# Kernel tuning notes

Measured on AMD Instinct MI355X. Metric: run time of the kernel, lower is better.

## Reference

```python
import jax, jax.numpy as jnp
import numpy as np

N_NODES = 50000


def _gcn_norm(edge_index, num_nodes):
    # PyG GCNConv default: add self-loops, symmetric normalization D^-1/2 A D^-1/2
    src, dst = edge_index[0], edge_index[1]
    loops = jnp.arange(num_nodes, dtype=src.dtype)
    src = jnp.concatenate([src, loops])
    dst = jnp.concatenate([dst, loops])
    deg = jax.ops.segment_sum(jnp.ones_like(src, dtype=jnp.float32), dst,
                              num_segments=num_nodes)
    dis = jnp.where(deg > 0, jax.lax.rsqrt(jnp.maximum(deg, 1.0)), 0.0)
    norm = dis[src] * dis[dst]  # [E']
    return src, dst, norm


def _gcn_conv(x, W, b, src, dst, norm, num_nodes):
    h = x @ W                                   # [N, out] transform first
    msg = h[src] * norm[:, None]                # [E', out] gather + scale
    agg = jax.ops.segment_sum(msg, dst, num_segments=num_nodes)  # scatter-add
    return agg + b


def setup_inputs() -> dict:
    key = jax.random.key(0)
    k1, k2, k3, k4 = jax.random.split(key, 4)
    n, e, d_in, d_h = N_NODES, 800000, 256, 128
    basic_block = jax.random.normal(k1, (n, d_in), dtype=jnp.float32)
    edge_index = jax.random.randint(k2, (2, e), 0, n, dtype=jnp.int64)
    W1 = jax.random.normal(k3, (d_in, d_h), dtype=jnp.float32) * (1.0 / np.sqrt(d_in))
    b1 = jnp.zeros((d_h,), dtype=jnp.float32)
    W2 = jax.random.normal(k4, (d_h, d_h), dtype=jnp.float32) * (1.0 / np.sqrt(d_h))
    b2 = jnp.zeros((d_h,), dtype=jnp.float32)
    return {"basic_block": basic_block, "edge_index": edge_index,
            "W1": W1, "b1": b1, "W2": W2, "b2": b2}


def reference(basic_block, edge_index, W1, b1, W2, b2):
    n = basic_block.shape[0]
    src, dst, norm = _gcn_norm(edge_index, n)
    x = jax.nn.relu(_gcn_conv(basic_block, W1, b1, src, dst, norm, n))
    x = _gcn_conv(x, W2, b2, src, dst, norm, n)
    return x
```

## Files before the change

### kernel.cpp

```cpp
#include <hip/hip_runtime.h>
#include <hip/hip_bf16.h>
#include <stdint.h>

#define D_H 128

typedef __bf16 bf16_t;
typedef unsigned short u16;
typedef bf16_t bf16x8 __attribute__((ext_vector_type(8)));
typedef bf16_t bf16x4 __attribute__((ext_vector_type(4)));
typedef float  f32x4  __attribute__((ext_vector_type(4)));

__global__ void k_countrank(const int* __restrict__ dst, int* __restrict__ cnt,
                            u16* __restrict__ rank, int E, int crBlocks,
                            const float* __restrict__ W1, bf16_t* __restrict__ W1h,
                            bf16_t* __restrict__ W1l, int K1,
                            const float* __restrict__ W2, bf16_t* __restrict__ W2h,
                            bf16_t* __restrict__ W2l, int K2) {
    if ((int)blockIdx.x < crBlocks) {
        int e = blockIdx.x * 256 + threadIdx.x;
        if (e < E) rank[e] = (u16)atomicAdd(&cnt[dst[e]], 1);
        return;
    }
    int id = ((int)blockIdx.x - crBlocks) * 256 + threadIdx.x;
    int n1 = K1 * 128;
    if (id < n1) {
        int k = id >> 7, n = id & 127;
        float w = W1[id];
        bf16_t h = (bf16_t)w;
        W1h[(size_t)n * K1 + k] = h;
        W1l[(size_t)n * K1 + k] = (bf16_t)(w - (float)h);
    } else if (id < n1 + K2 * 128) {
        int id2 = id - n1;
        int k = id2 >> 7, n = id2 & 127;
        float w = W2[id2];
        bf16_t h = (bf16_t)w;
        W2h[(size_t)n * K2 + k] = h;
        W2l[(size_t)n * K2 + k] = (bf16_t)(w - (float)h);
    }
}

__global__ __launch_bounds__(1024) void k_scan1(const int* __restrict__ cnt,
                                                int* __restrict__ out,
                                                int* __restrict__ bsums,
                                                float* __restrict__ dis, int N) {
    __shared__ int tmp[1024];
    int t = threadIdx.x;
    int i = blockIdx.x * 1024 + t;
    int v = (i < N) ? cnt[i] : 0;
    if (i < N) dis[i] = 1.0f / sqrtf((float)(v + 1));
    tmp[t] = v;
    __syncthreads();
    for (int d = 1; d < 1024; d <<= 1) {
        int x = (t >= d) ? tmp[t - d] : 0;
        __syncthreads();
        tmp[t] += x;
        __syncthreads();
    }
    if (i < N) out[i] = tmp[t] - v;
    if (t == 1023) bsums[blockIdx.x] = tmp[t];
}

__global__ void k_scan2(int* __restrict__ bsums, int nb) {
    __shared__ int tmp[64];
    int t = threadIdx.x;
    int v = (t < nb) ? bsums[t] : 0;
    tmp[t] = v;
    __syncthreads();
    for (int d = 1; d < 64; d <<= 1) {
        int x = (t >= d) ? tmp[t - d] : 0;
        __syncthreads();
        tmp[t] += x;
        __syncthreads();
    }
    if (t < nb) bsums[t] = tmp[t] - v;
}

__global__ __launch_bounds__(1024) void k_scan3(int* __restrict__ off,
                                                const int* __restrict__ bsums,
                                                int N, int E) {
    int i = blockIdx.x * 1024 + threadIdx.x;
    if (i < N) off[i] += bsums[blockIdx.x];
    if (i == 0) off[N] = E;
}

#define LDK 40
#define FILL_PER 2

__global__ __launch_bounds__(256) void k_mm1fill(
        const float* __restrict__ Af,
        const bf16_t* __restrict__ Wh, const bf16_t* __restrict__ Wl,
        const float* __restrict__ dis, bf16_t* __restrict__ Cb,
        int N, int K,
        const int* __restrict__ src, const int* __restrict__ dst,
        const int* __restrict__ off, const u16* __restrict__ rank,
        u16* __restrict__ csr16, int E, int totThreads) {
    __shared__ bf16_t AsH[64][LDK];
    __shared__ bf16_t AsL[64][LDK];
    __shared__ bf16_t BsH[64][LDK];
    __shared__ bf16_t BsL[64][LDK];

    const int t    = threadIdx.x;
    const int lane = t & 63;
    const int wave = t >> 6;
    const int row0 = ((int)blockIdx.x >> 1) * 64;
    const int col0 = ((int)blockIdx.x & 1) * 64;
    const int wm   = (wave & 1) * 32;
    const int wn   = (wave >> 1) * 32;
    const int fm   = lane & 15;
    const int fq   = lane >> 4;

    const int g = (int)blockIdx.x * 256 + t;
    int epos[FILL_PER];
    u16 esrc[FILL_PER];
#pragma unroll
    for (int i = 0; i < FILL_PER; i++) {
        int e = g + i * totThreads;
        if (e < E) {
            int d = dst[e];
            epos[i] = off[d] + (int)rank[e];
            esrc[i] = (u16)src[e];
        } else {
            epos[i] = -1;
            esrc[i] = 0;
        }
    }

    const int ar0 = t >> 3;
    const int ar1 = (t >> 3) + 32;
    const int ac4 = t & 7;
    const int br  = t >> 2;
    const int bc8 = t & 3;
    const int gr0 = row0 + ar0;
    const int gr1 = row0 + ar1;

    float4 rA0, rA1;
    bf16x8 rBh, rBl;
    const float4 fz = make_float4(0.f, 0.f, 0.f, 0.f);

    auto gload = [&](int k0) {
        rA0 = (gr0 < N) ? *(const float4*)(Af + (size_t)gr0 * K + k0 + ac4 * 4) : fz;
        rA1 = (gr1 < N) ? *(const float4*)(Af + (size_t)gr1 * K + k0 + ac4 * 4) : fz;
        rBh = *(const bf16x8*)(Wh + (size_t)(col0 + br) * K + k0 + bc8 * 8);
        rBl = *(const bf16x8*)(Wl + (size_t)(col0 + br) * K + k0 + bc8 * 8);
    };
    auto lstore = [&]() {
        float4 v = rA0;
        bf16_t h0 = (bf16_t)v.x, h1 = (bf16_t)v.y, h2 = (bf16_t)v.z, h3 = (bf16_t)v.w;
        *(bf16x4*)&AsH[ar0][ac4 * 4] = (bf16x4){h0, h1, h2, h3};
        *(bf16x4*)&AsL[ar0][ac4 * 4] = (bf16x4){(bf16_t)(v.x - (float)h0), (bf16_t)(v.y - (float)h1),
                                                (bf16_t)(v.z - (float)h2), (bf16_t)(v.w - (float)h3)};
        v = rA1;
        h0 = (bf16_t)v.x; h1 = (bf16_t)v.y; h2 = (bf16_t)v.z; h3 = (bf16_t)v.w;
        *(bf16x4*)&AsH[ar1][ac4 * 4] = (bf16x4){h0, h1, h2, h3};
        *(bf16x4*)&AsL[ar1][ac4 * 4] = (bf16x4){(bf16_t)(v.x - (float)h0), (bf16_t)(v.y - (float)h1),
                                                (bf16_t)(v.z - (float)h2), (bf16_t)(v.w - (float)h3)};
        *(bf16x8*)&BsH[br][bc8 * 8] = rBh;
        *(bf16x8*)&BsL[br][bc8 * 8] = rBl;
    };

    f32x4 acc[2][2] = {};

    gload(0);
    for (int k0 = 0; k0 < K; k0 += 32) {
        __syncthreads();
        lstore();
        if (k0 + 32 < K) gload(k0 + 32);
        __syncthreads();

        bf16x8 ah[2], al[2], bh[2], bl[2];
#pragma unroll
        for (int i = 0; i < 2; i++) {
            ah[i] = *(const bf16x8*)&AsH[wm + i * 16 + fm][fq * 8];
            al[i] = *(const bf16x8*)&AsL[wm + i * 16 + fm][fq * 8];
            bh[i] = *(const bf16x8*)&BsH[wn + i * 16 + fm][fq * 8];
            bl[i] = *(const bf16x8*)&BsL[wn + i * 16 + fm][fq * 8];
        }
#pragma unroll
        for (int mi = 0; mi < 2; mi++)
#pragma unroll
            for (int ni = 0; ni < 2; ni++) {
                acc[mi][ni] = __builtin_amdgcn_mfma_f32_16x16x32_bf16(ah[mi], bh[ni], acc[mi][ni], 0, 0, 0);
                acc[mi][ni] = __builtin_amdgcn_mfma_f32_16x16x32_bf16(ah[mi], bl[ni], acc[mi][ni], 0, 0, 0);
                acc[mi][ni] = __builtin_amdgcn_mfma_f32_16x16x32_bf16(al[mi], bh[ni], acc[mi][ni], 0, 0, 0);
            }
    }

#pragma unroll
    for (int mi = 0; mi < 2; mi++)
#pragma unroll
        for (int r = 0; r < 4; r++) {
            int grow = row0 + wm + mi * 16 + fq * 4 + r;
            if (grow < N) {
                float dr = dis[grow];
#pragma unroll
                for (int ni = 0; ni < 2; ni++)
                    Cb[(size_t)grow * D_H + col0 + wn + ni * 16 + fm] = (bf16_t)(dr * acc[mi][ni][r]);
            }
        }

#pragma unroll
    for (int i = 0; i < FILL_PER; i++)
        if (epos[i] >= 0) csr16[epos[i]] = esrc[i];
}

__global__ __launch_bounds__(256) void k_mm2(const bf16_t* __restrict__ Ah,
                                             const bf16_t* __restrict__ Al,
                                             const bf16_t* __restrict__ Wh,
                                             const bf16_t* __restrict__ Wl,
                                             const float* __restrict__ dis,
                                             bf16_t* __restrict__ Cb,
                                             int N, int K) {
    __shared__ bf16_t AsH[64][LDK];
    __shared__ bf16_t AsL[64][LDK];
    __shared__ bf16_t BsH[64][LDK];
    __shared__ bf16_t BsL[64][LDK];

    const int t    = threadIdx.x;
    const int lane = t & 63;
    const int wave = t >> 6;
    const int row0 = ((int)blockIdx.x >> 1) * 64;
    const int col0 = ((int)blockIdx.x & 1) * 64;
    const int wm   = (wave & 1) * 32;
    const int wn   = (wave >> 1) * 32;
    const int fm   = lane & 15;
    const int fq   = lane >> 4;

    const int r8  = t >> 2;
    const int c8  = t & 3;
    const int gr  = row0 + r8;

    bf16x8 rAh, rAl, rBh, rBl;
    auto gload = [&](int k0) {
        bf16x8 z = {};
        rAh = (gr < N) ? *(const bf16x8*)(Ah + (size_t)gr * K + k0 + c8 * 8) : z;
        rAl = (gr < N) ? *(const bf16x8*)(Al + (size_t)gr * K + k0 + c8 * 8) : z;
        rBh = *(const bf16x8*)(Wh + (size_t)(col0 + r8) * K + k0 + c8 * 8);
        rBl = *(const bf16x8*)(Wl + (size_t)(col0 + r8) * K + k0 + c8 * 8);
    };
    auto lstore = [&]() {
        *(bf16x8*)&AsH[r8][c8 * 8] = rAh;
        *(bf16x8*)&AsL[r8][c8 * 8] = rAl;
        *(bf16x8*)&BsH[r8][c8 * 8] = rBh;
        *(bf16x8*)&BsL[r8][c8 * 8] = rBl;
    };

    f32x4 acc[2][2] = {};

    gload(0);
    for (int k0 = 0; k0 < K; k0 += 32) {
        __syncthreads();
        lstore();
        if (k0 + 32 < K) gload(k0 + 32);
        __syncthreads();

        bf16x8 ah[2], al[2], bh[2], bl[2];
#pragma unroll
        for (int i = 0; i < 2; i++) {
            ah[i] = *(const bf16x8*)&AsH[wm + i * 16 + fm][fq * 8];
            al[i] = *(const bf16x8*)&AsL[wm + i * 16 + fm][fq * 8];
            bh[i] = *(const bf16x8*)&BsH[wn + i * 16 + fm][fq * 8];
            bl[i] = *(const bf16x8*)&BsL[wn + i * 16 + fm][fq * 8];
        }
#pragma unroll
        for (int mi = 0; mi < 2; mi++)
#pragma unroll
            for (int ni = 0; ni < 2; ni++) {
                acc[mi][ni] = __builtin_amdgcn_mfma_f32_16x16x32_bf16(ah[mi], bh[ni], acc[mi][ni], 0, 0, 0);
                acc[mi][ni] = __builtin_amdgcn_mfma_f32_16x16x32_bf16(ah[mi], bl[ni], acc[mi][ni], 0, 0, 0);
                acc[mi][ni] = __builtin_amdgcn_mfma_f32_16x16x32_bf16(al[mi], bh[ni], acc[mi][ni], 0, 0, 0);
            }
    }

#pragma unroll
    for (int mi = 0; mi < 2; mi++)
#pragma unroll
        for (int r = 0; r < 4; r++) {
            int grow = row0 + wm + mi * 16 + fq * 4 + r;
            if (grow < N) {
                float dr = dis[grow];
#pragma unroll
                for (int ni = 0; ni < 2; ni++)
                    Cb[(size_t)grow * D_H + col0 + wn + ni * 16 + fm] = (bf16_t)(dr * acc[mi][ni][r]);
            }
        }
}

__global__ __launch_bounds__(256) void k_agg(const bf16_t* __restrict__ Hb,
                                             const float* __restrict__ dis,
                                             const int* __restrict__ off,
                                             const u16* __restrict__ csr16,
                                             const float4* __restrict__ bias4,
                                             float4* __restrict__ outF,
                                             bf16_t* __restrict__ outH,
                                             bf16_t* __restrict__ outL,
                                             int N, int mode) {
    const int slot = threadIdx.x >> 4;
    const int lane = threadIdx.x & 15;
    const int node = blockIdx.x * 16 + slot;
    if (node >= N) return;

    const bf16_t* Hrow = Hb + (size_t)lane * 8;

    float a0[8], a1[8], a2[8], a3[8];
    {
        bf16x8 v = *(const bf16x8*)(Hrow + (size_t)node * D_H);
#pragma unroll
        for (int j = 0; j < 8; j++) { a0[j] = (float)v[j]; a1[j] = 0.f; a2[j] = 0.f; a3[j] = 0.f; }
    }

    int p  = off[node];
    int p1 = off[node + 1];

    for (; p + 4 <= p1; p += 4) {
        int s0 = (int)csr16[p + 0], s1 = (int)csr16[p + 1];
        int s2 = (int)csr16[p + 2], s3 = (int)csr16[p + 3];
        bf16x8 h0 = *(const bf16x8*)(Hrow + (size_t)s0 * D_H);
        bf16x8 h1 = *(const bf16x8*)(Hrow + (size_t)s1 * D_H);
        bf16x8 h2 = *(const bf16x8*)(Hrow + (size_t)s2 * D_H);
        bf16x8 h3 = *(const bf16x8*)(Hrow + (size_t)s3 * D_H);
#pragma unroll
        for (int j = 0; j < 8; j++) {
            a0[j] += (float)h0[j];
            a1[j] += (float)h1[j];
            a2[j] += (float)h2[j];
            a3[j] += (float)h3[j];
        }
    }
    if (p + 2 <= p1) {
        int s0 = (int)csr16[p + 0], s1 = (int)csr16[p + 1];
        bf16x8 h0 = *(const bf16x8*)(Hrow + (size_t)s0 * D_H);
        bf16x8 h1 = *(const bf16x8*)(Hrow + (size_t)s1 * D_H);
#pragma unroll
        for (int j = 0; j < 8; j++) { a0[j] += (float)h0[j]; a1[j] += (float)h1[j]; }
        p += 2;
    }
    if (p < p1) {
        int s0 = (int)csr16[p];
        bf16x8 h0 = *(const bf16x8*)(Hrow + (size_t)s0 * D_H);
#pragma unroll
        for (int j = 0; j < 8; j++) a2[j] += (float)h0[j];
    }

    float sum[8];
#pragma unroll
    for (int j = 0; j < 8; j++) sum[j] = (a0[j] + a1[j]) + (a2[j] + a3[j]);

    const float  di = dis[node];
    const float4 b0 = bias4[lane * 2];
    const float4 b1 = bias4[lane * 2 + 1];
    float v0 = fmaf(di, sum[0], b0.x), v1 = fmaf(di, sum[1], b0.y);
    float v2 = fmaf(di, sum[2], b0.z), v3 = fmaf(di, sum[3], b0.w);
    float v4 = fmaf(di, sum[4], b1.x), v5 = fmaf(di, sum[5], b1.y);
    float v6 = fmaf(di, sum[6], b1.z), v7 = fmaf(di, sum[7], b1.w);

    if (mode == 1) {
        v0 = fmaxf(v0, 0.f); v1 = fmaxf(v1, 0.f); v2 = fmaxf(v2, 0.f); v3 = fmaxf(v3, 0.f);
        v4 = fmaxf(v4, 0.f); v5 = fmaxf(v5, 0.f); v6 = fmaxf(v6, 0.f); v7 = fmaxf(v7, 0.f);
        bf16_t h0 = (bf16_t)v0, h1 = (bf16_t)v1, h2 = (bf16_t)v2, h3 = (bf16_t)v3;
        bf16_t h4 = (bf16_t)v4, h5 = (bf16_t)v5, h6 = (bf16_t)v6, h7 = (bf16_t)v7;
        *(bf16x8*)(outH + (size_t)node * D_H + lane * 8) =
            (bf16x8){h0, h1, h2, h3, h4, h5, h6, h7};
        *(bf16x8*)(outL + (size_t)node * D_H + lane * 8) =
            (bf16x8){(bf16_t)(v0 - (float)h0), (bf16_t)(v1 - (float)h1),
                     (bf16_t)(v2 - (float)h2), (bf16_t)(v3 - (float)h3),
                     (bf16_t)(v4 - (float)h4), (bf16_t)(v5 - (float)h5),
                     (bf16_t)(v6 - (float)h6), (bf16_t)(v7 - (float)h7)};
    } else {
        outF[(size_t)node * 32 + lane * 2]     = make_float4(v0, v1, v2, v3);
        outF[(size_t)node * 32 + lane * 2 + 1] = make_float4(v4, v5, v6, v7);
    }
}

extern "C" void kernel_launch(void* const* d_in, const int* in_sizes, int n_in,
                              void* d_out, int out_size, void* d_ws, size_t ws_size,
                              hipStream_t stream) {
    const float* X  = (const float*)d_in[0];
    const int*   ei = (const int*)d_in[1];
    const float* W1 = (const float*)d_in[2];
    const float* b1 = (const float*)d_in[3];
    const float* W2 = (const float*)d_in[4];
    const float* b2 = (const float*)d_in[5];
    float* out = (float*)d_out;

    const int N  = in_sizes[0] / 256;
    const int E  = in_sizes[1] / 2;
    const int K1 = 256;

    const int* src = ei;
    const int* dst = ei + E;

    uintptr_t p = (uintptr_t)d_ws;
    auto carve = [&](size_t bytes) {
        uintptr_t q = p;
        p += (bytes + 255) & ~(size_t)255;
        return q;
    };
    int*    cnt   = (int*)carve((size_t)N * 4);
    int*    off   = (int*)carve((size_t)(N + 1) * 4);
    int*    bsums = (int*)carve(64 * 4);
    float*  dis   = (float*)carve((size_t)N * 4);
    u16*    rank  = (u16*)carve((size_t)E * 2);
    u16*    csr16 = (u16*)carve((size_t)E * 2);
    bf16_t* Hb    = (bf16_t*)carve((size_t)N * D_H * 2);
    bf16_t* X1h   = (bf16_t*)carve((size_t)N * D_H * 2);
    bf16_t* X1l   = (bf16_t*)carve((size_t)N * D_H * 2);
    bf16_t* W1h   = (bf16_t*)carve((size_t)K1 * D_H * 2);
    bf16_t* W1l   = (bf16_t*)carve((size_t)K1 * D_H * 2);
    bf16_t* W2h   = (bf16_t*)carve((size_t)D_H * D_H * 2);
    bf16_t* W2l   = (bf16_t*)carve((size_t)D_H * D_H * 2);

    const int nb = (N + 1023) / 1024;

    hipMemsetAsync(cnt, 0, (size_t)N * 4, stream);
    const int gcr   = (E + 255) / 256;
    const int gprep = (K1 * 128 + D_H * 128 + 255) / 256;
    k_countrank<<<gcr + gprep, 256, 0, stream>>>(dst, cnt, rank, E, gcr,
                                                 W1, W1h, W1l, K1,
                                                 W2, W2h, W2l, D_H);
    k_scan1<<<nb, 1024, 0, stream>>>(cnt, off, bsums, dis, N);
    k_scan2<<<1, 64, 0, stream>>>(bsums, nb);
    k_scan3<<<nb, 1024, 0, stream>>>(off, bsums, N, E);

    const int gmm = ((N + 63) / 64) * 2;
    const int gag = (N + 15) / 16;

    k_mm1fill<<<gmm, 256, 0, stream>>>(X, W1h, W1l, dis, Hb, N, K1,
                                       src, dst, off, rank, csr16, E, gmm * 256);
    k_agg<<<gag, 256, 0, stream>>>(Hb, dis, off, csr16,
                                   (const float4*)b1, nullptr, X1h, X1l, N, 1);

    k_mm2<<<gmm, 256, 0, stream>>>(X1h, X1l, W2h, W2l, dis, Hb, N, D_H);
    k_agg<<<gag, 256, 0, stream>>>(Hb, dis, off, csr16,
                                   (const float4*)b2, (float4*)out, nullptr, nullptr, N, 0);
}
```

Measured before the change: 269.5 us.

## Split degree counters into four copies and drop register prefetch in GEMMs

Spreads the edge-degree atomics across four counter copies, selected by block index, so atomics on the same node contend less. The scan sums the four copies, and a per-copy offset table is built so the CSR fill can place each edge correctly. Separately, both GEMM kernels drop register double-buffering of the global tiles and now load straight into LDS each iteration, which lowers register pressure but no longer overlaps the loads with compute. The cost is extra memory traffic for the memset and the offset arrays, plus an additional offset table.

```diff
diff --git a/kernel.cpp b/kernel.cpp
--- a/kernel.cpp
+++ b/kernel.cpp
@@ -10,18 +10,22 @@
 typedef bf16_t bf16x4 __attribute__((ext_vector_type(4)));
 typedef float  f32x4  __attribute__((ext_vector_type(4)));
 
-__global__ void k_countrank(const int* __restrict__ dst, int* __restrict__ cnt,
-                            u16* __restrict__ rank, int E, int crBlocks,
-                            const float* __restrict__ W1, bf16_t* __restrict__ W1h,
-                            bf16_t* __restrict__ W1l, int K1,
-                            const float* __restrict__ W2, bf16_t* __restrict__ W2h,
-                            bf16_t* __restrict__ W2l, int K2) {
-    if ((int)blockIdx.x < crBlocks) {
-        int e = blockIdx.x * 256 + threadIdx.x;
-        if (e < E) rank[e] = (u16)atomicAdd(&cnt[dst[e]], 1);
+__global__ void k_pre(const int* __restrict__ dst, int* __restrict__ cnt4,
+                      u16* __restrict__ rank, int E, int Nn, int gcr,
+                      const float* __restrict__ W1, bf16_t* __restrict__ W1h,
+                      bf16_t* __restrict__ W1l, int K1,
+                      const float* __restrict__ W2, bf16_t* __restrict__ W2h,
+                      bf16_t* __restrict__ W2l, int K2) {
+    int bx = (int)blockIdx.x;
+    if (bx < gcr) {
+        int e = bx * 256 + threadIdx.x;
+        if (e < E) {
+            int d = dst[e];
+            rank[e] = (u16)atomicAdd(&cnt4[(bx & 3) * Nn + d], 1);
+        }
         return;
     }
-    int id = ((int)blockIdx.x - crBlocks) * 256 + threadIdx.x;
+    int id = (bx - gcr) * 256 + threadIdx.x;
     int n1 = K1 * 128;
     if (id < n1) {
         int k = id >> 7, n = id & 127;
@@ -39,15 +43,18 @@
     }
 }
 
-__global__ __launch_bounds__(1024) void k_scan1(const int* __restrict__ cnt,
+__global__ __launch_bounds__(1024) void k_scan1(const int* __restrict__ cnt4,
                                                 int* __restrict__ out,
                                                 int* __restrict__ bsums,
                                                 float* __restrict__ dis, int N) {
     __shared__ int tmp[1024];
     int t = threadIdx.x;
     int i = blockIdx.x * 1024 + t;
-    int v = (i < N) ? cnt[i] : 0;
-    if (i < N) dis[i] = 1.0f / sqrtf((float)(v + 1));
+    int v = 0;
+    if (i < N) {
+        v = cnt4[i] + cnt4[N + i] + cnt4[2 * N + i] + cnt4[3 * N + i];
+        dis[i] = 1.0f / sqrtf((float)(v + 1));
+    }
     tmp[t] = v;
     __syncthreads();
     for (int d = 1; d < 1024; d <<= 1) {
@@ -77,9 +84,19 @@
 
 __global__ __launch_bounds__(1024) void k_scan3(int* __restrict__ off,
                                                 const int* __restrict__ bsums,
+                                                const int* __restrict__ cnt4,
+                                                int* __restrict__ offc,
                                                 int N, int E) {
     int i = blockIdx.x * 1024 + threadIdx.x;
-    if (i < N) off[i] += bsums[blockIdx.x];
+    if (i < N) {
+        int o = off[i] + bsums[blockIdx.x];
+        off[i] = o;
+        int c0 = cnt4[i], c1 = cnt4[N + i], c2 = cnt4[2 * N + i];
+        offc[i]         = o;
+        offc[N + i]     = o + c0;
+        offc[2 * N + i] = o + c0 + c1;
+        offc[3 * N + i] = o + c0 + c1 + c2;
+    }
     if (i == 0) off[N] = E;
 }
 
@@ -92,7 +109,7 @@
         const float* __restrict__ dis, bf16_t* __restrict__ Cb,
         int N, int K,
         const int* __restrict__ src, const int* __restrict__ dst,
-        const int* __restrict__ off, const u16* __restrict__ rank,
+        const int* __restrict__ offc, const u16* __restrict__ rank,
         u16* __restrict__ csr16, int E, int totThreads) {
     __shared__ bf16_t AsH[64][LDK];
     __shared__ bf16_t AsL[64][LDK];
@@ -116,8 +133,9 @@
     for (int i = 0; i < FILL_PER; i++) {
         int e = g + i * totThreads;
         if (e < E) {
-            int d = dst[e];
-            epos[i] = off[d] + (int)rank[e];
+            int d    = dst[e];
+            int copy = (e >> 8) & 3;
+            epos[i] = offc[copy * N + d] + (int)rank[e];
             esrc[i] = (u16)src[e];
         } else {
             epos[i] = -1;
@@ -125,46 +143,32 @@
         }
     }
 
-    const int ar0 = t >> 3;
-    const int ar1 = (t >> 3) + 32;
-    const int ac4 = t & 7;
-    const int br  = t >> 2;
-    const int bc8 = t & 3;
-    const int gr0 = row0 + ar0;
-    const int gr1 = row0 + ar1;
-
-    float4 rA0, rA1;
-    bf16x8 rBh, rBl;
-    const float4 fz = make_float4(0.f, 0.f, 0.f, 0.f);
-
-    auto gload = [&](int k0) {
-        rA0 = (gr0 < N) ? *(const float4*)(Af + (size_t)gr0 * K + k0 + ac4 * 4) : fz;
-        rA1 = (gr1 < N) ? *(const float4*)(Af + (size_t)gr1 * K + k0 + ac4 * 4) : fz;
-        rBh = *(const bf16x8*)(Wh + (size_t)(col0 + br) * K + k0 + bc8 * 8);
-        rBl = *(const bf16x8*)(Wl + (size_t)(col0 + br) * K + k0 + bc8 * 8);
-    };
-    auto lstore = [&]() {
-        float4 v = rA0;
-        bf16_t h0 = (bf16_t)v.x, h1 = (bf16_t)v.y, h2 = (bf16_t)v.z, h3 = (bf16_t)v.w;
-        *(bf16x4*)&AsH[ar0][ac4 * 4] = (bf16x4){h0, h1, h2, h3};
-        *(bf16x4*)&AsL[ar0][ac4 * 4] = (bf16x4){(bf16_t)(v.x - (float)h0), (bf16_t)(v.y - (float)h1),
-                                                (bf16_t)(v.z - (float)h2), (bf16_t)(v.w - (float)h3)};
-        v = rA1;
-        h0 = (bf16_t)v.x; h1 = (bf16_t)v.y; h2 = (bf16_t)v.z; h3 = (bf16_t)v.w;
-        *(bf16x4*)&AsH[ar1][ac4 * 4] = (bf16x4){h0, h1, h2, h3};
-        *(bf16x4*)&AsL[ar1][ac4 * 4] = (bf16x4){(bf16_t)(v.x - (float)h0), (bf16_t)(v.y - (float)h1),
-                                                (bf16_t)(v.z - (float)h2), (bf16_t)(v.w - (float)h3)};
-        *(bf16x8*)&BsH[br][bc8 * 8] = rBh;
-        *(bf16x8*)&BsL[br][bc8 * 8] = rBl;
-    };
-
     f32x4 acc[2][2] = {};
 
-    gload(0);
     for (int k0 = 0; k0 < K; k0 += 32) {
         __syncthreads();
-        lstore();
-        if (k0 + 32 < K) gload(k0 + 32);
+#pragma unroll
+        for (int i = 0; i < 2; i++) {
+            int idx = t + i * 256;
+            int r   = idx >> 3;
+            int c4  = idx & 7;
+            int gr  = row0 + r;
+            float4 v = make_float4(0.f, 0.f, 0.f, 0.f);
+            if (gr < N) v = *(const float4*)(Af + (size_t)gr * K + k0 + c4 * 4);
+            bf16_t h0 = (bf16_t)v.x, h1 = (bf16_t)v.y, h2 = (bf16_t)v.z, h3 = (bf16_t)v.w;
+            bf16_t l0 = (bf16_t)(v.x - (float)h0);
+            bf16_t l1 = (bf16_t)(v.y - (float)h1);
+            bf16_t l2 = (bf16_t)(v.z - (float)h2);
+            bf16_t l3 = (bf16_t)(v.w - (float)h3);
+            *(bf16x4*)&AsH[r][c4 * 4] = (bf16x4){h0, h1, h2, h3};
+            *(bf16x4*)&AsL[r][c4 * 4] = (bf16x4){l0, l1, l2, l3};
+        }
+        {
+            int r  = t >> 2;
+            int c8 = t & 3;
+            *(bf16x8*)&BsH[r][c8 * 8] = *(const bf16x8*)(Wh + (size_t)(col0 + r) * K + k0 + c8 * 8);
+            *(bf16x8*)&BsL[r][c8 * 8] = *(const bf16x8*)(Wl + (size_t)(col0 + r) * K + k0 + c8 * 8);
+        }
         __syncthreads();
 
         bf16x8 ah[2], al[2], bh[2], bl[2];
@@ -225,32 +229,24 @@
     const int fm   = lane & 15;
     const int fq   = lane >> 4;
 
-    const int r8  = t >> 2;
-    const int c8  = t & 3;
-    const int gr  = row0 + r8;
-
-    bf16x8 rAh, rAl, rBh, rBl;
-    auto gload = [&](int k0) {
-        bf16x8 z = {};
-        rAh = (gr < N) ? *(const bf16x8*)(Ah + (size_t)gr * K + k0 + c8 * 8) : z;
-        rAl = (gr < N) ? *(const bf16x8*)(Al + (size_t)gr * K + k0 + c8 * 8) : z;
-        rBh = *(const bf16x8*)(Wh + (size_t)(col0 + r8) * K + k0 + c8 * 8);
-        rBl = *(const bf16x8*)(Wl + (size_t)(col0 + r8) * K + k0 + c8 * 8);
-    };
-    auto lstore = [&]() {
-        *(bf16x8*)&AsH[r8][c8 * 8] = rAh;
-        *(bf16x8*)&AsL[r8][c8 * 8] = rAl;
-        *(bf16x8*)&BsH[r8][c8 * 8] = rBh;
-        *(bf16x8*)&BsL[r8][c8 * 8] = rBl;
-    };
-
     f32x4 acc[2][2] = {};
 
-    gload(0);
     for (int k0 = 0; k0 < K; k0 += 32) {
         __syncthreads();
-        lstore();
-        if (k0 + 32 < K) gload(k0 + 32);
+        {
+            int r  = t >> 2;
+            int c8 = t & 3;
+            int gr = row0 + r;
+            bf16x8 vh = {}, vl = {};
+            if (gr < N) {
+                vh = *(const bf16x8*)(Ah + (size_t)gr * K + k0 + c8 * 8);
+                vl = *(const bf16x8*)(Al + (size_t)gr * K + k0 + c8 * 8);
+            }
+            *(bf16x8*)&AsH[r][c8 * 8] = vh;
+            *(bf16x8*)&AsL[r][c8 * 8] = vl;
+            *(bf16x8*)&BsH[r][c8 * 8] = *(const bf16x8*)(Wh + (size_t)(col0 + r) * K + k0 + c8 * 8);
+            *(bf16x8*)&BsL[r][c8 * 8] = *(const bf16x8*)(Wl + (size_t)(col0 + r) * K + k0 + c8 * 8);
+        }
         __syncthreads();
 
         bf16x8 ah[2], al[2], bh[2], bl[2];
@@ -395,8 +391,9 @@
         p += (bytes + 255) & ~(size_t)255;
         return q;
     };
-    int*    cnt   = (int*)carve((size_t)N * 4);
+    int*    cnt4  = (int*)carve((size_t)N * 4 * 4);
     int*    off   = (int*)carve((size_t)(N + 1) * 4);
+    int*    offc  = (int*)carve((size_t)N * 4 * 4);
     int*    bsums = (int*)carve(64 * 4);
     float*  dis   = (float*)carve((size_t)N * 4);
     u16*    rank  = (u16*)carve((size_t)E * 2);
@@ -411,21 +408,21 @@
 
     const int nb = (N + 1023) / 1024;
 
-    hipMemsetAsync(cnt, 0, (size_t)N * 4, stream);
-    const int gcr   = (E + 255) / 256;
-    const int gprep = (K1 * 128 + D_H * 128 + 255) / 256;
-    k_countrank<<<gcr + gprep, 256, 0, stream>>>(dst, cnt, rank, E, gcr,
-                                                 W1, W1h, W1l, K1,
-                                                 W2, W2h, W2l, D_H);
-    k_scan1<<<nb, 1024, 0, stream>>>(cnt, off, bsums, dis, N);
+    hipMemsetAsync(cnt4, 0, (size_t)N * 4 * 4, stream);
+    const int gcr = (E + 255) / 256;
+    const int gw  = (K1 * 128 + D_H * 128 + 255) / 256;
+    k_pre<<<gcr + gw, 256, 0, stream>>>(dst, cnt4, rank, E, N, gcr,
+                                        W1, W1h, W1l, K1,
+                                        W2, W2h, W2l, D_H);
+    k_scan1<<<nb, 1024, 0, stream>>>(cnt4, off, bsums, dis, N);
     k_scan2<<<1, 64, 0, stream>>>(bsums, nb);
-    k_scan3<<<nb, 1024, 0, stream>>>(off, bsums, N, E);
+    k_scan3<<<nb, 1024, 0, stream>>>(off, bsums, cnt4, offc, N, E);
 
     const int gmm = ((N + 63) / 64) * 2;
     const int gag = (N + 15) / 16;
 
     k_mm1fill<<<gmm, 256, 0, stream>>>(X, W1h, W1l, dis, Hb, N, K1,
-                                       src, dst, off, rank, csr16, E, gmm * 256);
+                                       src, dst, offc, rank, csr16, E, gmm * 256);
     k_agg<<<gag, 256, 0, stream>>>(Hb, dis, off, csr16,
                                    (const float4*)b1, nullptr, X1h, X1l, N, 1);
 
```

After: 250.1 us. 1.08x faster.
